# Performance work log

Measured on AMD Instinct MI355X. Metric: run time of the kernel, lower is better.

The kernel has to match this reference:

```python
import jax, jax.numpy as jnp
import numpy as np

B, N, F_IN, F_OUT, H = 4, 2048, 256, 256, 4
NEG_INF = -1e9
EDGE_PROB = 0.05
LEAKY_SLOPE = 0.2  # tf.nn.leaky_relu default alpha


def setup_inputs() -> dict:
    key = jax.random.key(0)
    k_x, k_m, k_w, k_a, k_b = jax.random.split(key, 5)
    inputs = jax.random.normal(k_x, (B, N, F_IN), dtype=jnp.float32)
    # bias: additive adjacency mask, 0 on edges / -1e9 off-edges (standard GAT)
    u = jax.random.uniform(k_m, (B, N, N), dtype=jnp.float32)
    bias = jnp.where(u < EDGE_PROB, 0.0, NEG_INF).astype(jnp.float32)
    # self-loops so every softmax row has at least one valid entry
    bias = bias.at[:, jnp.arange(N), jnp.arange(N)].set(0.0)
    # per-head learned params (uniform [0,1) init as in the original)
    W = jax.random.uniform(k_w, (H, F_IN, F_OUT), dtype=jnp.float32)
    a = jax.random.uniform(k_a, (H, F_OUT), dtype=jnp.float32)
    b = jax.random.uniform(k_b, (H, F_OUT), dtype=jnp.float32)
    return {"inputs": inputs, "bias": bias, "W": W, "a": a, "b": b}


def reference(inputs, bias, W, a, b):
    # transformed: [H, B, N, F_OUT]
    t = jnp.einsum('bnf,hfo->hbno', inputs, W) + b[:, None, None, :]
    # per-node score s = t @ a : [H, B, N]
    s = jnp.einsum('hbno,ho->hbn', t, a)
    # weights[i,j] = s[i] + s[j]  (weights + transpose)
    w = s[..., :, None] + s[..., None, :]  # [H, B, N, N]
    coefs = jax.nn.softmax(jax.nn.leaky_relu(w, negative_slope=LEAKY_SLOPE) + bias, axis=-1)
    heads = jnp.einsum('hbnm,hbmo->hbno', coefs, t)  # [H, B, N, F_OUT]
    return jnp.mean(heads, axis=0)  # (1/num_heads) * add_n(heads)
```

## Files before the change

kernel.cpp:

```cpp
#include <hip/hip_runtime.h>
#include <hip/hip_bf16.h>
#include <stdint.h>

#define H 4
#define BB 4
#define NN 2048
#define FIN 256
#define FOUT 256
#define M_TOT (BB*NN)
#define LOG2E 1.44269504f

typedef float f32x4 __attribute__((ext_vector_type(4)));
typedef short s16x8 __attribute__((ext_vector_type(8)));
typedef unsigned int u32;

static __device__ __forceinline__ short f2bf(float f) {
    return __builtin_bit_cast(short, __float2bfloat16(f));
}
static __device__ __forceinline__ float bf2f(short u) {
    unsigned x = ((unsigned)(unsigned short)u) << 16;
    return __builtin_bit_cast(float, x);
}

__global__ __launch_bounds__(256) void k_prep(const float* __restrict__ W, const float* __restrict__ a,
                                              const float* __restrict__ bvec,
                                              short* __restrict__ WT, float* __restrict__ q,
                                              float* __restrict__ c) {
    int bid = blockIdx.x;
    if (bid < 64) {
        __shared__ float lds[64][65];
        int h = bid >> 4, kt = (bid >> 2) & 3, ot = bid & 3;
        int kb = kt * 64, ob = ot * 64;
        int tx = threadIdx.x & 63, ty = threadIdx.x >> 6;
#pragma unroll
        for (int r = 0; r < 16; ++r) {
            int k_l = ty + r * 4;
            lds[tx][k_l] = W[(size_t)(h * FIN + kb + k_l) * FOUT + ob + tx];
        }
        __syncthreads();
#pragma unroll
        for (int r = 0; r < 16; ++r) {
            int o_l = ty + r * 4;
            WT[(size_t)(h * FOUT + ob + o_l) * FIN + kb + tx] = f2bf(lds[o_l][tx]);
        }
    } else if (bid < 320) {
        int wv = ((bid - 64) * 256 + threadIdx.x) >> 6;
        int lane = threadIdx.x & 63;
        int h = wv >> 8, f = wv & 255;
        float4 w4 = *(const float4*)(W + (size_t)(h * FIN + f) * FOUT + lane * 4);
        float4 a4 = *(const float4*)(a + h * FOUT + lane * 4);
        float d = w4.x * a4.x + w4.y * a4.y + w4.z * a4.z + w4.w * a4.w;
#pragma unroll
        for (int off = 32; off; off >>= 1) d += __shfl_xor(d, off);
        if (lane == 0) q[h * FIN + f] = d;
    } else {
        int h = threadIdx.x >> 6, lane = threadIdx.x & 63;
        float4 b4 = *(const float4*)(bvec + h * FOUT + lane * 4);
        float4 a4 = *(const float4*)(a + h * FOUT + lane * 4);
        float d = b4.x * a4.x + b4.y * a4.y + b4.z * a4.z + b4.w * a4.w;
#pragma unroll
        for (int off = 32; off; off >>= 1) d += __shfl_xor(d, off);
        if (lane == 0) c[h] = d;
    }
}

__global__ __launch_bounds__(256) void k_s(const float* __restrict__ X, const float* __restrict__ q,
                                           const float* __restrict__ c, float* __restrict__ s,
                                           short* __restrict__ Xbf) {
    int m = blockIdx.x * 4 + (threadIdx.x >> 6);
    int lane = threadIdx.x & 63;
    float4 xv = *(const float4*)(X + (size_t)m * FIN + lane * 4);
    short4 xb;
    xb.x = f2bf(xv.x); xb.y = f2bf(xv.y); xb.z = f2bf(xv.z); xb.w = f2bf(xv.w);
    *(short4*)(Xbf + (size_t)m * FIN + lane * 4) = xb;
#pragma unroll
    for (int h = 0; h < H; ++h) {
        float4 qv = *(const float4*)(q + h * FIN + lane * 4);
        float d = xv.x * qv.x + xv.y * qv.y + xv.z * qv.z + xv.w * qv.w;
#pragma unroll
        for (int off = 32; off; off >>= 1) d += __shfl_xor(d, off);
        if (lane == 0) s[h * M_TOT + m] = d + c[h];
    }
}

__global__ __launch_bounds__(256) void k_maskmax(const float* __restrict__ bias, const float* __restrict__ s,
                                                 unsigned* __restrict__ mask, float* __restrict__ mx) {
    __shared__ float sl[8192];
    int tid = threadIdx.x;
    int row0 = blockIdx.x * 4;
    int b = row0 >> 11;
#pragma unroll
    for (int i = 0; i < 8; ++i) {
        int flat = i * 1024 + tid * 4;
        int h = flat >> 11, j = flat & 2047;
        float4 v = *(const float4*)(s + (size_t)h * M_TOT + (size_t)b * NN + j);
        int phys = flat ^ (((flat >> 5) & 7) << 2);
        *(float4*)(sl + phys) = v;
    }
    __syncthreads();

    int w = tid >> 6, lane = tid & 63;
    int row = row0 + w;
    const float* bp = bias + (size_t)row * NN + lane * 32;
    unsigned bits = 0;
#pragma unroll
    for (int k = 0; k < 8; ++k) {
        float4 v = *(const float4*)(bp + k * 4);
        bits |= (v.x > -1.f ? 1u : 0u) << (k * 4 + 0);
        bits |= (v.y > -1.f ? 1u : 0u) << (k * 4 + 1);
        bits |= (v.z > -1.f ? 1u : 0u) << (k * 4 + 2);
        bits |= (v.w > -1.f ? 1u : 0u) << (k * 4 + 3);
    }
    mask[(size_t)row * 64 + lane] = bits;
#pragma unroll
    for (int h = 0; h < H; ++h) {
        float m = -3e38f;
#pragma unroll
        for (int k = 0; k < 8; ++k) {
            int flat = h * 2048 + lane * 32 + k * 4;
            int phys = flat ^ (((flat >> 5) & 7) << 2);
            float4 sv = *(const float4*)(sl + phys);
            m = fmaxf(m, ((bits >> (k * 4 + 0)) & 1u) ? sv.x : -3e38f);
            m = fmaxf(m, ((bits >> (k * 4 + 1)) & 1u) ? sv.y : -3e38f);
            m = fmaxf(m, ((bits >> (k * 4 + 2)) & 1u) ? sv.z : -3e38f);
            m = fmaxf(m, ((bits >> (k * 4 + 3)) & 1u) ? sv.w : -3e38f);
        }
#pragma unroll
        for (int off = 32; off; off >>= 1) m = fmaxf(m, __shfl_xor(m, off));
        if (lane == 0) mx[h * M_TOT + row] = m;
    }
}

__global__ __launch_bounds__(256) void k_gemm_t(const short* __restrict__ WT, const short* __restrict__ Xbf,
                                                const float* __restrict__ bvec, short* __restrict__ tTs) {
    __shared__ short ot[64][136];
    int h = blockIdx.z;
    int ob = blockIdx.y * 64;
    int mb = blockIdx.x * 128;
    int tid = threadIdx.x;
    int lane = tid & 63, w = tid >> 6;
    int r16 = lane & 15, g = lane >> 4;
    int mw = mb + w * 32;
    f32x4 acc[4][2] = {};
    for (int k = 0; k < FIN; k += 32) {
        s16x8 afr[4], bfr[2];
#pragma unroll
        for (int fa = 0; fa < 4; ++fa)
            afr[fa] = *(const s16x8*)(WT + (size_t)(h * FOUT + ob + fa * 16 + r16) * FIN + k + g * 8);
#pragma unroll
        for (int fb = 0; fb < 2; ++fb)
            bfr[fb] = *(const s16x8*)(Xbf + (size_t)(mw + fb * 16 + r16) * FIN + k + g * 8);
#pragma unroll
        for (int fa = 0; fa < 4; ++fa)
#pragma unroll
            for (int fb = 0; fb < 2; ++fb)
                acc[fa][fb] = __builtin_amdgcn_mfma_f32_16x16x32_bf16(afr[fa], bfr[fb], acc[fa][fb], 0, 0, 0);
    }
#pragma unroll
    for (int fa = 0; fa < 4; ++fa) {
#pragma unroll
        for (int r = 0; r < 4; ++r) {
            int o_l = fa * 16 + g * 4 + r;
            float bv = bvec[h * FOUT + ob + o_l];
#pragma unroll
            for (int fb = 0; fb < 2; ++fb)
                ot[o_l][w * 32 + fb * 16 + r16] = f2bf(acc[fa][fb][r] + bv);
        }
    }
    __syncthreads();
    int bb = mb >> 11, jloc = mb & 2047;
    int jt0 = jloc >> 6;
    size_t slab = (size_t)((h * 4 + bb) * 32) * 16384;
#pragma unroll
    for (int cc = 0; cc < 4; ++cc) {
        int sid = cc * 256 + tid;
        int frag = sid >> 6;
        int l = sid & 63;
        int f_l = frag >> 2, jt_sel = (frag >> 1) & 1, par = frag & 1;
        int o_l = f_l * 16 + (l & 15);
        int m_l = jt_sel * 64 + par * 32 + (l >> 4) * 8;
        s16x8 v = *(const s16x8*)&ot[o_l][m_l];
        int fid = ((ob >> 4) + f_l) * 2 + par;
        size_t addr = slab + (size_t)(jt0 + jt_sel) * 16384 + fid * 512 + l * 8;
        *(s16x8*)(tTs + addr) = v;
    }
}

__global__ __launch_bounds__(512, 4) void k_attn(const short* __restrict__ tTs, const float* __restrict__ s,
                                                 const unsigned* __restrict__ mask, const float* __restrict__ mx,
                                                 short* __restrict__ OTn) {
    __shared__ short smem[34048];

    int flat = blockIdx.x + 32 * (blockIdx.y + 4 * blockIdx.z);
    int swz = (flat & 7) * 64 + (flat >> 3);
    int qt = swz & 31, b = (swz >> 5) & 3, h = swz >> 7;
    int ib = qt * 64;

    int tid = threadIdx.x;
    int lane = tid & 63, w = tid >> 6;
    int r16 = lane & 15, g = lane >> 4;
    int par = w & 1, oh = w >> 1;
    size_t gm = (size_t)b * NN;

    const short* slab = tTs + (size_t)((h * 4 + b) * 32) * 16384;
    const float* srow = s + h * M_TOT + gm;

    int i = ib + oh * 16 + r16;
    float si = srow[i];
    float mxi = mx[h * M_TOT + gm + i];
    float z = si + mxi;
    float Mlog = fmaxf(z, 0.2f * z) * LOG2E;
    float siL = si * LOG2E;
    float c1 = siL - Mlog;
    float c2 = 0.2f * siL - Mlog;
    const float k1 = LOG2E, k2 = 0.2f * LOG2E;
    const unsigned* mk = mask + (gm + i) * 64;

    int chk = ((((par << 2) + g) ^ (r16 & 7)) << 3);
    int rdP = r16 * 64 + chk;
    int wrP = oh * 1024 + rdP;

    f32x4 acc[4][4] = {};
    float lsum = 0.f;

    s16x8 acur[4], anext[4];
#pragma unroll
    for (int f = 0; f < 4; ++f)
        acur[f] = *(const s16x8*)(slab + ((oh * 4 + f) * 2 + par) * 512 + lane * 8);

    float4 psj0, psj1; unsigned pwm;
    {
        int jw = par * 32;
        psj0 = *(const float4*)(srow + jw + g * 8);
        psj1 = *(const float4*)(srow + jw + g * 8 + 4);
        pwm = mk[par];
    }

    for (int t = 0; t < 32; ++t) {
        if (t < 31) {
            const short* tp = slab + (size_t)(t + 1) * 16384;
#pragma unroll
            for (int f = 0; f < 4; ++f)
                anext[f] = *(const s16x8*)(tp + ((oh * 4 + f) * 2 + par) * 512 + lane * 8);
        }

        float sjv[8] = {psj0.x, psj0.y, psj0.z, psj0.w, psj1.x, psj1.y, psj1.z, psj1.w};
        unsigned bb0 = pwm >> (g * 8);
        s16x8 pb;
#pragma unroll
        for (int e = 0; e < 8; ++e) {
            float u = fmaf(sjv[e], k1, c1);
            float vv = fmaf(sjv[e], k2, c2);
            float aa = fmaxf(u, vv);
            aa = ((bb0 >> e) & 1u) ? aa : -200.f;
            float p = __builtin_amdgcn_exp2f(aa);
            lsum += p;
            pb[e] = f2bf(p);
        }
        *(s16x8*)(smem + (t & 1) * 4096 + wrP) = pb;

        if (t < 31) {
            int jw = (t + 1) * 64 + par * 32;
            psj0 = *(const float4*)(srow + jw + g * 8);
            psj1 = *(const float4*)(srow + jw + g * 8 + 4);
            pwm = mk[(t + 1) * 2 + par];
        }

        asm volatile("s_waitcnt lgkmcnt(0)" ::: "memory");
        __builtin_amdgcn_sched_barrier(0);
        __builtin_amdgcn_s_barrier();
        __builtin_amdgcn_sched_barrier(0);

        const short* Pb = smem + (t & 1) * 4096;
        __builtin_amdgcn_s_setprio(1);
#pragma unroll
        for (int qf = 0; qf < 4; ++qf) {
            s16x8 pf = *(const s16x8*)(Pb + qf * 1024 + rdP);
            acc[0][qf] = __builtin_amdgcn_mfma_f32_16x16x32_bf16(acur[0], pf, acc[0][qf], 0, 0, 0);
            acc[1][qf] = __builtin_amdgcn_mfma_f32_16x16x32_bf16(acur[1], pf, acc[1][qf], 0, 0, 0);
            acc[2][qf] = __builtin_amdgcn_mfma_f32_16x16x32_bf16(acur[2], pf, acc[2][qf], 0, 0, 0);
            acc[3][qf] = __builtin_amdgcn_mfma_f32_16x16x32_bf16(acur[3], pf, acc[3][qf], 0, 0, 0);
        }
        __builtin_amdgcn_s_setprio(0);

        if (t < 31) {
#pragma unroll
            for (int f = 0; f < 4; ++f) acur[f] = anext[f];
        }
    }

    __syncthreads();
    lsum += __shfl_xor(lsum, 16);
    lsum += __shfl_xor(lsum, 32);
    float* pl    = (float*)((char*)smem + 67584);
    float* plinv = pl + 64;
    if (par == 1 && g == 0) pl[oh * 16 + r16] = lsum;
    __syncthreads();
    if (par == 0 && g == 0) plinv[oh * 16 + r16] = 1.f / (lsum + pl[oh * 16 + r16]);
    __syncthreads();
    float linv[4];
#pragma unroll
    for (int qf = 0; qf < 4; ++qf) linv[qf] = plinv[qf * 16 + r16];

    float* exf  = (float*)smem;
    short* outT = smem + 16896;
#pragma unroll
    for (int rnd = 0; rnd < 2; ++rnd) {
        if (par == 1 && (oh >> 1) == rnd) {
#pragma unroll
            for (int f = 0; f < 4; ++f)
#pragma unroll
                for (int qf = 0; qf < 4; ++qf) {
                    int irow = qf * 16 + r16;
                    int o_loc = (oh & 1) * 64 + f * 16 + g * 4;
                    *(f32x4*)(exf + irow * 132 + o_loc) = acc[f][qf];
                }
        }
        __syncthreads();
        if (par == 0 && (oh >> 1) == rnd) {
#pragma unroll
            for (int f = 0; f < 4; ++f)
#pragma unroll
                for (int qf = 0; qf < 4; ++qf) {
                    int irow = qf * 16 + r16;
                    int o_loc = (oh & 1) * 64 + f * 16 + g * 4;
                    f32x4 v = acc[f][qf] + *(const f32x4*)(exf + irow * 132 + o_loc);
                    short4 o4;
                    o4.x = f2bf(v[0] * linv[qf]); o4.y = f2bf(v[1] * linv[qf]);
                    o4.z = f2bf(v[2] * linv[qf]); o4.w = f2bf(v[3] * linv[qf]);
                    *(short4*)(outT + irow * 264 + rnd * 128 + o_loc) = o4;
                }
        }
        __syncthreads();
    }

    {
        int row = tid >> 3, col = (tid & 7) * 32;
        const short* src = outT + row * 264 + col;
        size_t gdst = ((size_t)h * M_TOT + gm + ib + row) * 256 + col;
#pragma unroll
        for (int cc = 0; cc < 4; ++cc)
            *(s16x8*)(OTn + gdst + cc * 8) = *(const s16x8*)(src + cc * 8);
    }
}

__global__ __launch_bounds__(256) void k_reduce(const short* __restrict__ OTn, float* __restrict__ out) {
    size_t idx = ((size_t)blockIdx.x * 256 + threadIdx.x) * 8;
    float acc[8] = {};
#pragma unroll
    for (int h = 0; h < H; ++h) {
        s16x8 v = *(const s16x8*)(OTn + (size_t)h * M_TOT * 256 + idx);
#pragma unroll
        for (int e = 0; e < 8; ++e) acc[e] += bf2f(v[e]);
    }
    float4 o0, o1;
    o0.x = acc[0] * 0.25f; o0.y = acc[1] * 0.25f; o0.z = acc[2] * 0.25f; o0.w = acc[3] * 0.25f;
    o1.x = acc[4] * 0.25f; o1.y = acc[5] * 0.25f; o1.z = acc[6] * 0.25f; o1.w = acc[7] * 0.25f;
    *(float4*)(out + idx) = o0;
    *(float4*)(out + idx + 4) = o1;
}

extern "C" void kernel_launch(void* const* d_in, const int* in_sizes, int n_in,
                              void* d_out, int out_size, void* d_ws, size_t ws_size,
                              hipStream_t stream) {
    const float* X    = (const float*)d_in[0];
    const float* bias = (const float*)d_in[1];
    const float* W    = (const float*)d_in[2];
    const float* a    = (const float*)d_in[3];
    const float* bvec = (const float*)d_in[4];
    float* out = (float*)d_out;

    char* ws = (char*)d_ws;
    short*    Xbf  = (short*)ws;
    short*    WT   = (short*)(ws + (4u << 20));
    float*    q    = (float*)(ws + (4u << 20) + (768u << 10));
    float*    c    = q + H * FIN;
    float*    s    = (float*)(ws + (5u << 20));
    float*    mxp  = (float*)(ws + (5u << 20) + (256u << 10));
    short*    tTs  = (short*)(ws + (6u << 20));
    short*    OTn  = (short*)(ws + (22u << 20));
    unsigned* mask = (unsigned*)(ws + (38u << 20));

    k_prep<<<321, 256, 0, stream>>>(W, a, bvec, WT, q, c);
    k_s<<<2048, 256, 0, stream>>>(X, q, c, s, Xbf);
    k_maskmax<<<2048, 256, 0, stream>>>(bias, s, mask, mxp);
    k_gemm_t<<<dim3(64, 4, 4), 256, 0, stream>>>(WT, Xbf, bvec, tTs);
    k_attn<<<dim3(32, 4, 4), 512, 0, stream>>>(tTs, s, mask, mxp, OTn);
    k_reduce<<<1024, 256, 0, stream>>>(OTn, out);
}
```

Baseline: 117.3 us.

## Restructure attention kernel to 4 waves with per-wave query rows and no LDS P exchange

The attention kernel drops from 8 waves per block to 4. Each wave now owns 32 query rows and 128 output columns, and computes its own softmax probabilities directly in registers as the MFMA B operand. This removes the per-iteration LDS staging of P, the block barrier, and the cross-wave partial-sum reduction at the end. The trade-off is more exp work per wave, since P is recomputed by both column-half waves, along with more registers (8x2 accumulators) and fewer waves to hide memory latency.

```diff
diff --git a/kernel.cpp b/kernel.cpp
--- a/kernel.cpp
+++ b/kernel.cpp
@@ -186,10 +186,10 @@
     }
 }
 
-__global__ __launch_bounds__(512, 4) void k_attn(const short* __restrict__ tTs, const float* __restrict__ s,
+__global__ __launch_bounds__(256, 2) void k_attn(const short* __restrict__ tTs, const float* __restrict__ s,
                                                  const unsigned* __restrict__ mask, const float* __restrict__ mx,
                                                  short* __restrict__ OTn) {
-    __shared__ short smem[34048];
+    __shared__ short outT[64 * 264];
 
     int flat = blockIdx.x + 32 * (blockIdx.y + 4 * blockIdx.z);
     int swz = (flat & 7) * 64 + (flat >> 3);
@@ -198,148 +198,109 @@
 
     int tid = threadIdx.x;
     int lane = tid & 63, w = tid >> 6;
-    int r16 = lane & 15, g = lane >> 4;
-    int par = w & 1, oh = w >> 1;
+    int l15 = lane & 15, g = lane >> 4;
+    int wq = w & 1, wo = w >> 1;
+    int wo8 = wo * 8;
     size_t gm = (size_t)b * NN;
 
     const short* slab = tTs + (size_t)((h * 4 + b) * 32) * 16384;
     const float* srow = s + h * M_TOT + gm;
 
-    int i = ib + oh * 16 + r16;
-    float si = srow[i];
-    float mxi = mx[h * M_TOT + gm + i];
-    float z = si + mxi;
-    float Mlog = fmaxf(z, 0.2f * z) * LOG2E;
-    float siL = si * LOG2E;
-    float c1 = siL - Mlog;
-    float c2 = 0.2f * siL - Mlog;
+    int qb = ib + wq * 32;
+    int q0 = qb + l15, q1 = q0 + 16;
+    float si0 = srow[q0], si1 = srow[q1];
+    float mx0 = mx[h * M_TOT + gm + q0];
+    float mx1 = mx[h * M_TOT + gm + q1];
+    float z0 = si0 + mx0, z1 = si1 + mx1;
+    float M0 = fmaxf(z0, 0.2f * z0) * LOG2E;
+    float M1 = fmaxf(z1, 0.2f * z1) * LOG2E;
+    float c10 = si0 * LOG2E - M0, c20 = 0.2f * si0 * LOG2E - M0;
+    float c11 = si1 * LOG2E - M1, c21 = 0.2f * si1 * LOG2E - M1;
     const float k1 = LOG2E, k2 = 0.2f * LOG2E;
-    const unsigned* mk = mask + (gm + i) * 64;
-
-    int chk = ((((par << 2) + g) ^ (r16 & 7)) << 3);
-    int rdP = r16 * 64 + chk;
-    int wrP = oh * 1024 + rdP;
-
-    f32x4 acc[4][4] = {};
-    float lsum = 0.f;
-
-    s16x8 acur[4], anext[4];
-#pragma unroll
-    for (int f = 0; f < 4; ++f)
-        acur[f] = *(const s16x8*)(slab + ((oh * 4 + f) * 2 + par) * 512 + lane * 8);
-
-    float4 psj0, psj1; unsigned pwm;
+    const unsigned* mk0 = mask + (gm + q0) * 64;
+    const unsigned* mk1 = mask + (gm + q1) * 64;
+    int go8 = g * 8;
+
+    f32x4 acc[8][2] = {};
+    float lsum0 = 0.f, lsum1 = 0.f;
+
+    s16x8 acu[8], anx[8];
+#pragma unroll
+    for (int f = 0; f < 8; ++f)
+        acu[f] = *(const s16x8*)(slab + ((wo8 + f) * 2 + 0) * 512 + lane * 8);
+    float4 csj0 = *(const float4*)(srow + go8);
+    float4 csj1 = *(const float4*)(srow + go8 + 4);
+    unsigned cw0 = mk0[0], cw1 = mk1[0];
+
+    for (int t = 0; t < 64; ++t) {
+        float4 nsj0, nsj1; unsigned nw0, nw1;
+        if (t < 63) {
+            const short* tp = slab + (size_t)((t + 1) >> 1) * 16384;
+            int pr = (t + 1) & 1;
+#pragma unroll
+            for (int f = 0; f < 8; ++f)
+                anx[f] = *(const s16x8*)(tp + ((wo8 + f) * 2 + pr) * 512 + lane * 8);
+            nsj0 = *(const float4*)(srow + (t + 1) * 32 + go8);
+            nsj1 = *(const float4*)(srow + (t + 1) * 32 + go8 + 4);
+            nw0 = mk0[t + 1];
+            nw1 = mk1[t + 1];
+        }
+
+        float sjv[8] = {csj0.x, csj0.y, csj0.z, csj0.w, csj1.x, csj1.y, csj1.z, csj1.w};
+        unsigned b0 = cw0 >> go8, b1 = cw1 >> go8;
+        s16x8 pb0, pb1;
+#pragma unroll
+        for (int e = 0; e < 8; ++e) {
+            float sj = sjv[e];
+            float u0 = fmaf(sj, k1, c10), v0 = fmaf(sj, k2, c20);
+            float a0 = fmaxf(u0, v0);
+            a0 = ((b0 >> e) & 1u) ? a0 : -200.f;
+            float p0 = __builtin_amdgcn_exp2f(a0);
+            lsum0 += p0;
+            pb0[e] = f2bf(p0);
+            float u1 = fmaf(sj, k1, c11), v1 = fmaf(sj, k2, c21);
+            float a1 = fmaxf(u1, v1);
+            a1 = ((b1 >> e) & 1u) ? a1 : -200.f;
+            float p1 = __builtin_amdgcn_exp2f(a1);
+            lsum1 += p1;
+            pb1[e] = f2bf(p1);
+        }
+
+#pragma unroll
+        for (int f = 0; f < 8; ++f) {
+            acc[f][0] = __builtin_amdgcn_mfma_f32_16x16x32_bf16(acu[f], pb0, acc[f][0], 0, 0, 0);
+            acc[f][1] = __builtin_amdgcn_mfma_f32_16x16x32_bf16(acu[f], pb1, acc[f][1], 0, 0, 0);
+        }
+
+        if (t < 63) {
+#pragma unroll
+            for (int f = 0; f < 8; ++f) acu[f] = anx[f];
+            csj0 = nsj0; csj1 = nsj1; cw0 = nw0; cw1 = nw1;
+        }
+    }
+
+    lsum0 += __shfl_xor(lsum0, 16); lsum0 += __shfl_xor(lsum0, 32);
+    lsum1 += __shfl_xor(lsum1, 16); lsum1 += __shfl_xor(lsum1, 32);
+    float linv0 = 1.f / lsum0, linv1 = 1.f / lsum1;
+
+#pragma unroll
+    for (int f = 0; f < 8; ++f) {
+        int col = wo * 128 + f * 16 + g * 4;
+        short4 o0, o1;
+        o0.x = f2bf(acc[f][0][0] * linv0); o0.y = f2bf(acc[f][0][1] * linv0);
+        o0.z = f2bf(acc[f][0][2] * linv0); o0.w = f2bf(acc[f][0][3] * linv0);
+        o1.x = f2bf(acc[f][1][0] * linv1); o1.y = f2bf(acc[f][1][1] * linv1);
+        o1.z = f2bf(acc[f][1][2] * linv1); o1.w = f2bf(acc[f][1][3] * linv1);
+        *(short4*)(&outT[(wq * 32 + l15) * 264 + col]) = o0;
+        *(short4*)(&outT[(wq * 32 + 16 + l15) * 264 + col]) = o1;
+    }
+    __syncthreads();
     {
-        int jw = par * 32;
-        psj0 = *(const float4*)(srow + jw + g * 8);
-        psj1 = *(const float4*)(srow + jw + g * 8 + 4);
-        pwm = mk[par];
-    }
-
-    for (int t = 0; t < 32; ++t) {
-        if (t < 31) {
-            const short* tp = slab + (size_t)(t + 1) * 16384;
-#pragma unroll
-            for (int f = 0; f < 4; ++f)
-                anext[f] = *(const s16x8*)(tp + ((oh * 4 + f) * 2 + par) * 512 + lane * 8);
-        }
-
-        float sjv[8] = {psj0.x, psj0.y, psj0.z, psj0.w, psj1.x, psj1.y, psj1.z, psj1.w};
-        unsigned bb0 = pwm >> (g * 8);
-        s16x8 pb;
-#pragma unroll
-        for (int e = 0; e < 8; ++e) {
-            float u = fmaf(sjv[e], k1, c1);
-            float vv = fmaf(sjv[e], k2, c2);
-            float aa = fmaxf(u, vv);
-            aa = ((bb0 >> e) & 1u) ? aa : -200.f;
-            float p = __builtin_amdgcn_exp2f(aa);
-            lsum += p;
-            pb[e] = f2bf(p);
-        }
-        *(s16x8*)(smem + (t & 1) * 4096 + wrP) = pb;
-
-        if (t < 31) {
-            int jw = (t + 1) * 64 + par * 32;
-            psj0 = *(const float4*)(srow + jw + g * 8);
-            psj1 = *(const float4*)(srow + jw + g * 8 + 4);
-            pwm = mk[(t + 1) * 2 + par];
-        }
-
-        asm volatile("s_waitcnt lgkmcnt(0)" ::: "memory");
-        __builtin_amdgcn_sched_barrier(0);
-        __builtin_amdgcn_s_barrier();
-        __builtin_amdgcn_sched_barrier(0);
-
-        const short* Pb = smem + (t & 1) * 4096;
-        __builtin_amdgcn_s_setprio(1);
-#pragma unroll
-        for (int qf = 0; qf < 4; ++qf) {
-            s16x8 pf = *(const s16x8*)(Pb + qf * 1024 + rdP);
-            acc[0][qf] = __builtin_amdgcn_mfma_f32_16x16x32_bf16(acur[0], pf, acc[0][qf], 0, 0, 0);
-            acc[1][qf] = __builtin_amdgcn_mfma_f32_16x16x32_bf16(acur[1], pf, acc[1][qf], 0, 0, 0);
-            acc[2][qf] = __builtin_amdgcn_mfma_f32_16x16x32_bf16(acur[2], pf, acc[2][qf], 0, 0, 0);
-            acc[3][qf] = __builtin_amdgcn_mfma_f32_16x16x32_bf16(acur[3], pf, acc[3][qf], 0, 0, 0);
-        }
-        __builtin_amdgcn_s_setprio(0);
-
-        if (t < 31) {
-#pragma unroll
-            for (int f = 0; f < 4; ++f) acur[f] = anext[f];
-        }
-    }
-
-    __syncthreads();
-    lsum += __shfl_xor(lsum, 16);
-    lsum += __shfl_xor(lsum, 32);
-    float* pl    = (float*)((char*)smem + 67584);
-    float* plinv = pl + 64;
-    if (par == 1 && g == 0) pl[oh * 16 + r16] = lsum;
-    __syncthreads();
-    if (par == 0 && g == 0) plinv[oh * 16 + r16] = 1.f / (lsum + pl[oh * 16 + r16]);
-    __syncthreads();
-    float linv[4];
-#pragma unroll
-    for (int qf = 0; qf < 4; ++qf) linv[qf] = plinv[qf * 16 + r16];
-
-    float* exf  = (float*)smem;
-    short* outT = smem + 16896;
-#pragma unroll
-    for (int rnd = 0; rnd < 2; ++rnd) {
-        if (par == 1 && (oh >> 1) == rnd) {
-#pragma unroll
-            for (int f = 0; f < 4; ++f)
-#pragma unroll
-                for (int qf = 0; qf < 4; ++qf) {
-                    int irow = qf * 16 + r16;
-                    int o_loc = (oh & 1) * 64 + f * 16 + g * 4;
-                    *(f32x4*)(exf + irow * 132 + o_loc) = acc[f][qf];
-                }
-        }
-        __syncthreads();
-        if (par == 0 && (oh >> 1) == rnd) {
-#pragma unroll
-            for (int f = 0; f < 4; ++f)
-#pragma unroll
-                for (int qf = 0; qf < 4; ++qf) {
-                    int irow = qf * 16 + r16;
-                    int o_loc = (oh & 1) * 64 + f * 16 + g * 4;
-                    f32x4 v = acc[f][qf] + *(const f32x4*)(exf + irow * 132 + o_loc);
-                    short4 o4;
-                    o4.x = f2bf(v[0] * linv[qf]); o4.y = f2bf(v[1] * linv[qf]);
-                    o4.z = f2bf(v[2] * linv[qf]); o4.w = f2bf(v[3] * linv[qf]);
-                    *(short4*)(outT + irow * 264 + rnd * 128 + o_loc) = o4;
-                }
-        }
-        __syncthreads();
-    }
-
-    {
-        int row = tid >> 3, col = (tid & 7) * 32;
-        const short* src = outT + row * 264 + col;
-        size_t gdst = ((size_t)h * M_TOT + gm + ib + row) * 256 + col;
-#pragma unroll
-        for (int cc = 0; cc < 4; ++cc)
+        int row = tid >> 2, off = (tid & 3) * 64;
+        size_t gdst = ((size_t)h * M_TOT + gm + ib + row) * 256 + off;
+        const short* src = &outT[row * 264 + off];
+#pragma unroll
+        for (int cc = 0; cc < 8; ++cc)
             *(s16x8*)(OTn + gdst + cc * 8) = *(const s16x8*)(src + cc * 8);
     }
 }
@@ -385,6 +346,6 @@
     k_s<<<2048, 256, 0, stream>>>(X, q, c, s, Xbf);
     k_maskmax<<<2048, 256, 0, stream>>>(bias, s, mask, mxp);
     k_gemm_t<<<dim3(64, 4, 4), 256, 0, stream>>>(WT, Xbf, bvec, tTs);
-    k_attn<<<dim3(32, 4, 4), 512, 0, stream>>>(tTs, s, mask, mxp, OTn);
+    k_attn<<<dim3(32, 4, 4), 256, 0, stream>>>(tTs, s, mask, mxp, OTn);
     k_reduce<<<1024, 256, 0, stream>>>(OTn, out);
 }
```

New measurement: 143.9 us. 22.6% more time.
